# Optimization experiments

Hardware: AMD Instinct MI355X
Metric: run time of the kernel (lower is better)

The kernel has to match this reference:

```python
import jax, jax.numpy as jnp
import numpy as np

N, E, DIN, H, C = 50000, 800000, 256, 4, 32  # nodes, edges, in_dim, heads, per-head dim
NEG_SLOPE = 0.2  # PyG GATConv default LeakyReLU slope


def setup_inputs() -> dict:
    key = jax.random.key(0)
    ks = jax.random.split(key, 12)
    x = jax.random.normal(ks[0], (N, DIN), jnp.float32)
    edge_index = jax.random.randint(ks[1], (2, E), 0, N, dtype=jnp.int64)
    # layer 1: in=DIN -> heads*C; layer 2: in=H*C -> heads*C (concat=True default)
    W1 = jax.random.normal(ks[2], (DIN, H * C), jnp.float32) / np.sqrt(DIN).astype(np.float32)
    as1 = jax.random.normal(ks[3], (H, C), jnp.float32) * 0.1
    ad1 = jax.random.normal(ks[4], (H, C), jnp.float32) * 0.1
    b1 = jnp.zeros((H * C,), jnp.float32)
    W2 = jax.random.normal(ks[5], (H * C, H * C), jnp.float32) / np.sqrt(H * C).astype(np.float32)
    as2 = jax.random.normal(ks[6], (H, C), jnp.float32) * 0.1
    ad2 = jax.random.normal(ks[7], (H, C), jnp.float32) * 0.1
    b2 = jnp.zeros((H * C,), jnp.float32)
    return {"x": x, "edge_index": edge_index, "W1": W1, "as1": as1, "ad1": ad1,
            "b1": b1, "W2": W2, "as2": as2, "ad2": ad2, "b2": b2}


def gat_conv(x, src, dst, W, a_src, a_dst, b):
    # x: [N, Fin] -> h: [N, H, C]
    n = x.shape[0]
    h = (x @ W).reshape(n, H, C)
    # per-node attention logits [N, H]
    e_src = jnp.einsum('nhc,hc->nh', h, a_src)
    e_dst = jnp.einsum('nhc,hc->nh', h, a_dst)
    # edge-wise logits + segment softmax over destination neighborhoods
    e = jax.nn.leaky_relu(e_src[src] + e_dst[dst], NEG_SLOPE)  # [Et, H]
    m = jax.ops.segment_max(e, dst, num_segments=n)
    ex = jnp.exp(e - m[dst])
    s = jax.ops.segment_sum(ex, dst, num_segments=n)
    alpha = ex / s[dst]  # self-loops guarantee every node has >=1 edge
    # weighted scatter-add aggregation
    out = jax.ops.segment_sum(h[src] * alpha[:, :, None], dst, num_segments=n)
    return out.reshape(n, H * C) + b


def reference(x, edge_index, W1, as1, ad1, b1, W2, as2, ad2, b2):
    n = x.shape[0]
    loop = jnp.arange(n, dtype=edge_index.dtype)
    src = jnp.concatenate([edge_index[0], loop])  # PyG GATConv adds self-loops
    dst = jnp.concatenate([edge_index[1], loop])
    h = jax.nn.elu(gat_conv(x, src, dst, W1, as1, ad1, b1))
    # dropout is a no-op in eval mode (F.dropout with training=False)
    out = jax.nn.elu(gat_conv(h, src, dst, W2, as2, ad2, b2))
    return out
```

## Files before the change

### kernel.cpp

```cpp
#include <hip/hip_runtime.h>
#include <hip/hip_fp16.h>
#include <type_traits>

#define NN 50000
#define NE 800000
#define ET (NE + NN)
#define NEG 0.2f
#define GGRID 782
#define EGRID 3321

typedef __attribute__((ext_vector_type(4))) float f32x4;
typedef __attribute__((ext_vector_type(8))) short s16x8;

#define GLD_LDS16(g, l)                                                        \
  __builtin_amdgcn_global_load_lds(                                            \
      (const __attribute__((address_space(1))) void*)(g),                      \
      (__attribute__((address_space(3))) void*)(l), 16, 0, 0)

__device__ __forceinline__ float lrelu(float x) { return x > 0.0f ? x : NEG * x; }
__device__ __forceinline__ float elu1(float x) { return x > 0.0f ? x : __expf(x) - 1.0f; }
__device__ __forceinline__ unsigned short f2bf(float f) {
  unsigned u = __float_as_uint(f);
  u += 0x7FFFu + ((u >> 16) & 1u);
  return (unsigned short)(u >> 16);
}
__device__ __forceinline__ float bf2f(unsigned short h) {
  return __uint_as_float(((unsigned)h) << 16);
}

__global__ void prep_count_kernel(const float* __restrict__ W1, short* __restrict__ W1h,
                                  short* __restrict__ W1l, const float* __restrict__ W2,
                                  short* __restrict__ W2h, short* __restrict__ W2l,
                                  const int* __restrict__ ei, int* __restrict__ cnt,
                                  int* __restrict__ rank) {
  if (blockIdx.x >= 192) {
    int e = (blockIdx.x - 192) * 256 + threadIdx.x;
    if (e >= ET) return;
    int dst = (e < NE) ? ei[NE + e] : (e - NE);
    rank[e] = atomicAdd(&cnt[dst], 1);
    return;
  }
  int idx = blockIdx.x * 256 + threadIdx.x;
  const float* W; short* Wth; short* Wtl; int Kdim;
  if (idx < 256 * 128) { W = W1; Wth = W1h; Wtl = W1l; Kdim = 256; }
  else {
    idx -= 256 * 128;
    W = W2; Wth = W2h; Wtl = W2l; Kdim = 128;
  }
  int k = idx >> 7, n = idx & 127;
  float w = W[idx];
  unsigned short h = f2bf(w);
  unsigned short l = f2bf(w - bf2f(h));
  Wth[n * Kdim + k] = (short)h;
  Wtl[n * Kdim + k] = (short)l;
}

template<int K, typename AT>
__global__ __launch_bounds__(256) void gemm_mfma(const AT* __restrict__ A,
                                                 const short* __restrict__ Bth,
                                                 const short* __restrict__ Btl,
                                                 const float* __restrict__ a_s,
                                                 const float* __restrict__ a_d,
                                                 __half* __restrict__ outh,
                                                 float* __restrict__ es,
                                                 float* __restrict__ ed,
                                                 const int* __restrict__ ei,
                                                 const int* __restrict__ rowp,
                                                 const int* __restrict__ rank,
                                                 int* __restrict__ colw) {
  if (blockIdx.x >= GGRID) {
    int e = (blockIdx.x - GGRID) * 256 + threadIdx.x;
    if (e < ET) {
      int src, dst;
      if (e < NE) { src = ei[e]; dst = ei[NE + e]; } else { src = dst = e - NE; }
      colw[rowp[dst] + rank[e]] = src;
    }
    return;
  }
  constexpr int NSTEP = K / 32;
  __shared__ short Ah[64 * 32], Al[64 * 32];
  __shared__ short Bh[128 * 32], Bl[128 * 32];
  const int tid = threadIdx.x;
  const int lane = tid & 63;
  const int wv = tid >> 6;
  const int wm = wv >> 1, wn = wv & 1;
  const int row0 = blockIdx.x * 64;
  const int srow = tid >> 2;
  const int skc = tid & 3;

  f32x4 acc[2][4];
#pragma unroll
  for (int i = 0; i < 2; ++i)
#pragma unroll
    for (int j = 0; j < 4; ++j) acc[i][j] = (f32x4){0.f, 0.f, 0.f, 0.f};

  for (int s = 0; s < NSTEP; ++s) {
    __syncthreads();
    {
      int grow = row0 + srow; grow = grow < NN ? grow : NN - 1;
      const AT* ap = &A[(size_t)grow * K + s * 32 + skc * 8];
      float xs[8];
      if constexpr (std::is_same_v<AT, float>) {
        float4 x0 = *(const float4*)ap;
        float4 x1 = *(const float4*)(ap + 4);
        xs[0]=x0.x; xs[1]=x0.y; xs[2]=x0.z; xs[3]=x0.w;
        xs[4]=x1.x; xs[5]=x1.y; xs[6]=x1.z; xs[7]=x1.w;
      } else {
        int4 raw = *(const int4*)ap;
        const __half2* hv = (const __half2*)&raw;
#pragma unroll
        for (int q = 0; q < 4; ++q) {
          float2 f = __half22float2(hv[q]);
          xs[2 * q] = f.x; xs[2 * q + 1] = f.y;
        }
      }
      int hi[4], lo[4];
#pragma unroll
      for (int q = 0; q < 4; ++q) {
        unsigned short h0 = f2bf(xs[2 * q]);
        unsigned short l0 = f2bf(xs[2 * q] - bf2f(h0));
        unsigned short h1 = f2bf(xs[2 * q + 1]);
        unsigned short l1 = f2bf(xs[2 * q + 1] - bf2f(h1));
        hi[q] = (int)(((unsigned)h1 << 16) | h0);
        lo[q] = (int)(((unsigned)l1 << 16) | l0);
      }
      *(int4*)&Ah[srow * 32 + skc * 8] = make_int4(hi[0], hi[1], hi[2], hi[3]);
      *(int4*)&Al[srow * 32 + skc * 8] = make_int4(lo[0], lo[1], lo[2], lo[3]);
    }
#pragma unroll
    for (int rr = 0; rr < 2; ++rr) {
      int n = srow + rr * 64;
      const short* gh = &Bth[(size_t)n * K + s * 32 + skc * 8];
      const short* gl = &Btl[(size_t)n * K + s * 32 + skc * 8];
      char* lbh = (char*)Bh + rr * 4096 + wv * 1024;
      char* lbl = (char*)Bl + rr * 4096 + wv * 1024;
      GLD_LDS16(gh, lbh);
      GLD_LDS16(gl, lbl);
    }
    __syncthreads();
    const int fr = lane & 15;
    const int fk = (lane >> 4) * 8;
    s16x8 ah[2], al[2], bh[4], bl[4];
#pragma unroll
    for (int mf = 0; mf < 2; ++mf) {
      int r = wm * 32 + mf * 16 + fr;
      ah[mf] = *(const s16x8*)&Ah[r * 32 + fk];
      al[mf] = *(const s16x8*)&Al[r * 32 + fk];
    }
#pragma unroll
    for (int nf = 0; nf < 4; ++nf) {
      int n = wn * 64 + nf * 16 + fr;
      bh[nf] = *(const s16x8*)&Bh[n * 32 + fk];
      bl[nf] = *(const s16x8*)&Bl[n * 32 + fk];
    }
#pragma unroll
    for (int mf = 0; mf < 2; ++mf)
#pragma unroll
      for (int nf = 0; nf < 4; ++nf) {
        acc[mf][nf] = __builtin_amdgcn_mfma_f32_16x16x32_bf16(ah[mf], bh[nf], acc[mf][nf], 0, 0, 0);
        acc[mf][nf] = __builtin_amdgcn_mfma_f32_16x16x32_bf16(ah[mf], bl[nf], acc[mf][nf], 0, 0, 0);
        acc[mf][nf] = __builtin_amdgcn_mfma_f32_16x16x32_bf16(al[mf], bh[nf], acc[mf][nf], 0, 0, 0);
      }
  }

  const int fr = lane & 15;
  const int fg = lane >> 4;
  float asr[4], adr[4];
#pragma unroll
  for (int nf = 0; nf < 4; ++nf) {
    int c = wn * 64 + nf * 16 + fr;
    asr[nf] = a_s[c]; adr[nf] = a_d[c];
  }
#pragma unroll
  for (int mf = 0; mf < 2; ++mf) {
#pragma unroll
    for (int r = 0; r < 4; ++r) {
      int row = row0 + wm * 32 + mf * 16 + fg * 4 + r;
      float sp0 = acc[mf][0][r] * asr[0] + acc[mf][1][r] * asr[1];
      float sp1 = acc[mf][2][r] * asr[2] + acc[mf][3][r] * asr[3];
      float dp0 = acc[mf][0][r] * adr[0] + acc[mf][1][r] * adr[1];
      float dp1 = acc[mf][2][r] * adr[2] + acc[mf][3][r] * adr[3];
#pragma unroll
      for (int off = 1; off < 16; off <<= 1) {
        sp0 += __shfl_xor(sp0, off); sp1 += __shfl_xor(sp1, off);
        dp0 += __shfl_xor(dp0, off); dp1 += __shfl_xor(dp1, off);
      }
      if (row < NN) {
#pragma unroll
        for (int nf = 0; nf < 4; ++nf)
          outh[(size_t)row * 128 + wn * 64 + nf * 16 + fr] = __float2half(acc[mf][nf][r]);
        if (fr == 0) {
          es[row * 4 + wn * 2 + 0] = sp0;
          es[row * 4 + wn * 2 + 1] = sp1;
          ed[row * 4 + wn * 2 + 0] = dp0;
          ed[row * 4 + wn * 2 + 1] = dp1;
        }
      }
    }
  }
}

__global__ __launch_bounds__(1024) void scan_kernel(const int* __restrict__ cnt,
                                                    int* __restrict__ row_ptr, int n) {
  __shared__ int wsum[16];
  __shared__ int blocktot_s;
  __shared__ int carry_s;
  const int lane = threadIdx.x & 63;
  const int wv = threadIdx.x >> 6;
  if (threadIdx.x == 0) carry_s = 0;
  __syncthreads();
  for (int base = 0; base < n; base += 4096) {
    int idx = base + threadIdx.x * 4;
    int4 v = {0, 0, 0, 0};
    if (idx < n) v = *(const int4*)&cnt[idx];
    int tsum = v.x + v.y + v.z + v.w;
    int sc = tsum;
#pragma unroll
    for (int off = 1; off < 64; off <<= 1) {
      int t = __shfl_up(sc, off);
      if (lane >= off) sc += t;
    }
    if (lane == 63) wsum[wv] = sc;
    __syncthreads();
    if (wv == 0 && lane < 16) {
      int ws = wsum[lane];
      int si = ws;
#pragma unroll
      for (int off = 1; off < 16; off <<= 1) {
        int t = __shfl_up(si, off);
        if (lane >= off) si += t;
      }
      wsum[lane] = si - ws;
      if (lane == 15) blocktot_s = si;
    }
    __syncthreads();
    int run = carry_s + wsum[wv] + (sc - tsum);
    if (idx < n) {
      int4 o;
      o.x = run; o.y = run + v.x; o.z = o.y + v.y; o.w = o.z + v.z;
      *(int4*)&row_ptr[idx] = o;
    }
    __syncthreads();
    if (threadIdx.x == 0) carry_s += blocktot_s;
    __syncthreads();
  }
  if (threadIdx.x == 0) row_ptr[n] = carry_s;
}

template<typename OT>
__global__ __launch_bounds__(128) void agg_fused(const __half* __restrict__ h,
                                                 const float4* __restrict__ es4,
                                                 const float4* __restrict__ ed4,
                                                 const int* __restrict__ row_ptr,
                                                 const int* __restrict__ col,
                                                 const float* __restrict__ bias,
                                                 OT* __restrict__ out) {
  __shared__ float wc[2][512];
  __shared__ int   cc[2][128];
  int wid = (blockIdx.x * 128 + threadIdx.x) >> 6;
  if (wid >= NN) return;
  const int lane = threadIdx.x & 63;
  const int wv = (threadIdx.x >> 6) & 1;
  const int start = row_ptr[wid], end = row_ptr[wid + 1];
  const int deg = end - start;
  const float4 edv = ed4[wid];
  const char* hb = (const char*)h;

  const bool v0 = lane < deg, v1 = lane + 64 < deg;
  int c0 = 0, c1 = 0;
  float4 e0, e1;
  if (v0) { c0 = col[start + lane]; e0 = es4[c0]; }
  if (v1) { c1 = col[start + lane + 64]; e1 = es4[c1]; }
  float s0 = 0.f, s1 = 0.f, s2 = 0.f, s3 = 0.f;
  float4 p0, p1;
  if (v0) {
    p0.x = __expf(lrelu(e0.x + edv.x)); p0.y = __expf(lrelu(e0.y + edv.y));
    p0.z = __expf(lrelu(e0.z + edv.z)); p0.w = __expf(lrelu(e0.w + edv.w));
    s0 += p0.x; s1 += p0.y; s2 += p0.z; s3 += p0.w;
  }
  if (v1) {
    p1.x = __expf(lrelu(e1.x + edv.x)); p1.y = __expf(lrelu(e1.y + edv.y));
    p1.z = __expf(lrelu(e1.z + edv.z)); p1.w = __expf(lrelu(e1.w + edv.w));
    s0 += p1.x; s1 += p1.y; s2 += p1.z; s3 += p1.w;
  }
  for (int j = start + lane + 128; j < end; j += 64) {
    float4 ev = es4[col[j]];
    s0 += __expf(lrelu(ev.x + edv.x)); s1 += __expf(lrelu(ev.y + edv.y));
    s2 += __expf(lrelu(ev.z + edv.z)); s3 += __expf(lrelu(ev.w + edv.w));
  }
#pragma unroll
  for (int off = 32; off; off >>= 1) {
    s0 += __shfl_xor(s0, off); s1 += __shfl_xor(s1, off);
    s2 += __shfl_xor(s2, off); s3 += __shfl_xor(s3, off);
  }
  const float i0 = 1.0f / s0, i1 = 1.0f / s1, i2 = 1.0f / s2, i3 = 1.0f / s3;
  if (v0) {
    float4 w; w.x = p0.x * i0; w.y = p0.y * i1; w.z = p0.z * i2; w.w = p0.w * i3;
    *(float4*)&wc[wv][lane * 4] = w;
    cc[wv][lane] = c0 << 8;
  }
  if (v1) {
    float4 w; w.x = p1.x * i0; w.y = p1.y * i1; w.z = p1.z * i2; w.w = p1.w * i3;
    *(float4*)&wc[wv][(lane + 64) * 4] = w;
    cc[wv][lane + 64] = c1 << 8;
  }
  const int deg1 = deg < 128 ? deg : 128;
  if (lane == 0 && (deg1 & 1)) {
    cc[wv][deg1] = cc[wv][0];
    float4 z = {0.f, 0.f, 0.f, 0.f};
    *(float4*)&wc[wv][deg1 * 4] = z;
  }

  const int half_ = lane >> 5;
  const int fl = lane & 31;
  const int hd2 = fl >> 3;
  const int fb = fl << 3;
  float a0 = 0.f, a1 = 0.f, a2 = 0.f, a3 = 0.f;
  const int degR = (deg1 + 1) & ~1;
  int jj = 0;
  for (; jj + 8 <= degR; jj += 8) {
    int off[4]; float w[4];
#pragma unroll
    for (int u = 0; u < 4; ++u) {
      int e = jj + 2 * u + half_;
      off[u] = cc[wv][e];
      w[u] = wc[wv][e * 4 + hd2];
    }
    int2 q[4];
#pragma unroll
    for (int u = 0; u < 4; ++u) q[u] = *(const int2*)(hb + off[u] + fb);
#pragma unroll
    for (int u = 0; u < 4; ++u) {
      float2 f0 = __half22float2(*(const __half2*)&q[u].x);
      float2 f1 = __half22float2(*(const __half2*)&q[u].y);
      a0 = fmaf(f0.x, w[u], a0); a1 = fmaf(f0.y, w[u], a1);
      a2 = fmaf(f1.x, w[u], a2); a3 = fmaf(f1.y, w[u], a3);
    }
  }
  for (; jj < degR; jj += 2) {
    int e = jj + half_;
    int off = cc[wv][e];
    float w = wc[wv][e * 4 + hd2];
    int2 q = *(const int2*)(hb + off + fb);
    float2 f0 = __half22float2(*(const __half2*)&q.x);
    float2 f1 = __half22float2(*(const __half2*)&q.y);
    a0 = fmaf(f0.x, w, a0); a1 = fmaf(f0.y, w, a1);
    a2 = fmaf(f1.x, w, a2); a3 = fmaf(f1.y, w, a3);
  }
  if (deg > 128) {
    float ih = hd2 == 0 ? i0 : hd2 == 1 ? i1 : hd2 == 2 ? i2 : i3;
    float eh = hd2 == 0 ? edv.x : hd2 == 1 ? edv.y : hd2 == 2 ? edv.z : edv.w;
    for (int j = start + 128 + half_; j < end; j += 2) {
      int t = col[j];
      const float* ep = (const float*)&es4[t];
      float w = __expf(lrelu(ep[hd2] + eh)) * ih;
      int2 q = *(const int2*)(hb + (t << 8) + fb);
      float2 f0 = __half22float2(*(const __half2*)&q.x);
      float2 f1 = __half22float2(*(const __half2*)&q.y);
      a0 = fmaf(f0.x, w, a0); a1 = fmaf(f0.y, w, a1);
      a2 = fmaf(f1.x, w, a2); a3 = fmaf(f1.y, w, a3);
    }
  }
  a0 += __shfl_xor(a0, 32); a1 += __shfl_xor(a1, 32);
  a2 += __shfl_xor(a2, 32); a3 += __shfl_xor(a3, 32);

  float4 bs = *(const float4*)&bias[fl * 4];
  if (half_ == 0) {
    float o0 = elu1(a0 + bs.x), o1 = elu1(a1 + bs.y);
    float o2 = elu1(a2 + bs.z), o3 = elu1(a3 + bs.w);
    if constexpr (std::is_same_v<OT, float>) {
      float4 o; o.x = o0; o.y = o1; o.z = o2; o.w = o3;
      *(float4*)&out[(size_t)wid * 128 + fl * 4] = o;
    } else {
      __half2 h01 = __floats2half2_rn(o0, o1);
      __half2 h23 = __floats2half2_rn(o2, o3);
      int2 pk; pk.x = *(int*)&h01; pk.y = *(int*)&h23;
      *(int2*)&out[(size_t)wid * 128 + fl * 4] = pk;
    }
  }
}

extern "C" void kernel_launch(void* const* d_in, const int* in_sizes, int n_in,
                              void* d_out, int out_size, void* d_ws, size_t ws_size,
                              hipStream_t stream) {
  const float* x   = (const float*)d_in[0];
  const int*   ei  = (const int*)d_in[1];
  const float* W1  = (const float*)d_in[2];
  const float* as1 = (const float*)d_in[3];
  const float* ad1 = (const float*)d_in[4];
  const float* b1  = (const float*)d_in[5];
  const float* W2  = (const float*)d_in[6];
  const float* as2 = (const float*)d_in[7];
  const float* ad2 = (const float*)d_in[8];
  const float* b2  = (const float*)d_in[9];

  char* ws = (char*)d_ws;
  __half* h     = (__half*)(ws);
  __half* h2    = (__half*)(ws + 12800000);
  float*  es    = (float*) (ws + 25600000);
  float*  ed    = (float*) (ws + 26400000);
  int*    cnt   = (int*)   (ws + 27200000);
  int*    rowp  = (int*)   (ws + 27400000);
  int*    col   = (int*)   (ws + 27600064);
  int*    rank  = (int*)   (ws + 31000064);
  short*  wt1h  = (short*) (ws + 34400064);
  short*  wt1l  = (short*) (ws + 34465600);
  short*  wt2h  = (short*) (ws + 34531136);
  short*  wt2l  = (short*) (ws + 34563904);

  hipMemsetAsync(cnt, 0, NN * sizeof(int), stream);

  prep_count_kernel<<<192 + EGRID, 256, 0, stream>>>(W1, wt1h, wt1l, W2, wt2h, wt2l,
                                                     ei, cnt, rank);

  scan_kernel<<<1, 1024, 0, stream>>>(cnt, rowp, NN);

  int ngrid = (NN + 1) / 2;

  gemm_mfma<256, float><<<GGRID + EGRID, 256, 0, stream>>>(
      x, wt1h, wt1l, as1, ad1, h, es, ed, ei, rowp, rank, col);

  agg_fused<__half><<<ngrid, 128, 0, stream>>>(h, (const float4*)es, (const float4*)ed,
                                               rowp, col, b1, h2);

  gemm_mfma<128, __half><<<GGRID, 256, 0, stream>>>(
      h2, wt2h, wt2l, as2, ad2, h, es, ed, nullptr, nullptr, nullptr, nullptr);
  agg_fused<float><<<ngrid, 128, 0, stream>>>(h, (const float4*)es, (const float4*)ed,
                                              rowp, col, b2, (float*)d_out);
}
```

Measured before the change: 181.5 us.

## Drop LDS staging in MFMA GEMM; each wave loads fragments directly from global

```diff
diff --git a/kernel.cpp b/kernel.cpp
--- a/kernel.cpp
+++ b/kernel.cpp
@@ -6,16 +6,11 @@
 #define NE 800000
 #define ET (NE + NN)
 #define NEG 0.2f
-#define GGRID 782
+#define GG2 1563
 #define EGRID 3321
 
 typedef __attribute__((ext_vector_type(4))) float f32x4;
 typedef __attribute__((ext_vector_type(8))) short s16x8;
-
-#define GLD_LDS16(g, l)                                                        \
-  __builtin_amdgcn_global_load_lds(                                            \
-      (const __attribute__((address_space(1))) void*)(g),                      \
-      (__attribute__((address_space(3))) void*)(l), 16, 0, 0)
 
 __device__ __forceinline__ float lrelu(float x) { return x > 0.0f ? x : NEG * x; }
 __device__ __forceinline__ float elu1(float x) { return x > 0.0f ? x : __expf(x) - 1.0f; }
@@ -68,8 +63,8 @@
                                                  const int* __restrict__ rowp,
                                                  const int* __restrict__ rank,
                                                  int* __restrict__ colw) {
-  if (blockIdx.x >= GGRID) {
-    int e = (blockIdx.x - GGRID) * 256 + threadIdx.x;
+  if (blockIdx.x >= GG2) {
+    int e = (blockIdx.x - GG2) * 256 + threadIdx.x;
     if (e < ET) {
       int src, dst;
       if (e < NE) { src = ei[e]; dst = ei[NE + e]; } else { src = dst = e - NE; }
@@ -78,93 +73,63 @@
     return;
   }
   constexpr int NSTEP = K / 32;
-  __shared__ short Ah[64 * 32], Al[64 * 32];
-  __shared__ short Bh[128 * 32], Bl[128 * 32];
   const int tid = threadIdx.x;
   const int lane = tid & 63;
-  const int wv = tid >> 6;
-  const int wm = wv >> 1, wn = wv & 1;
-  const int row0 = blockIdx.x * 64;
-  const int srow = tid >> 2;
-  const int skc = tid & 3;
-
-  f32x4 acc[2][4];
-#pragma unroll
-  for (int i = 0; i < 2; ++i)
-#pragma unroll
-    for (int j = 0; j < 4; ++j) acc[i][j] = (f32x4){0.f, 0.f, 0.f, 0.f};
-
-  for (int s = 0; s < NSTEP; ++s) {
-    __syncthreads();
-    {
-      int grow = row0 + srow; grow = grow < NN ? grow : NN - 1;
-      const AT* ap = &A[(size_t)grow * K + s * 32 + skc * 8];
-      float xs[8];
-      if constexpr (std::is_same_v<AT, float>) {
-        float4 x0 = *(const float4*)ap;
-        float4 x1 = *(const float4*)(ap + 4);
-        xs[0]=x0.x; xs[1]=x0.y; xs[2]=x0.z; xs[3]=x0.w;
-        xs[4]=x1.x; xs[5]=x1.y; xs[6]=x1.z; xs[7]=x1.w;
-      } else {
-        int4 raw = *(const int4*)ap;
-        const __half2* hv = (const __half2*)&raw;
-#pragma unroll
-        for (int q = 0; q < 4; ++q) {
-          float2 f = __half22float2(hv[q]);
-          xs[2 * q] = f.x; xs[2 * q + 1] = f.y;
-        }
-      }
-      int hi[4], lo[4];
-#pragma unroll
-      for (int q = 0; q < 4; ++q) {
-        unsigned short h0 = f2bf(xs[2 * q]);
-        unsigned short l0 = f2bf(xs[2 * q] - bf2f(h0));
-        unsigned short h1 = f2bf(xs[2 * q + 1]);
-        unsigned short l1 = f2bf(xs[2 * q + 1] - bf2f(h1));
-        hi[q] = (int)(((unsigned)h1 << 16) | h0);
-        lo[q] = (int)(((unsigned)l1 << 16) | l0);
-      }
-      *(int4*)&Ah[srow * 32 + skc * 8] = make_int4(hi[0], hi[1], hi[2], hi[3]);
-      *(int4*)&Al[srow * 32 + skc * 8] = make_int4(lo[0], lo[1], lo[2], lo[3]);
-    }
-#pragma unroll
-    for (int rr = 0; rr < 2; ++rr) {
-      int n = srow + rr * 64;
-      const short* gh = &Bth[(size_t)n * K + s * 32 + skc * 8];
-      const short* gl = &Btl[(size_t)n * K + s * 32 + skc * 8];
-      char* lbh = (char*)Bh + rr * 4096 + wv * 1024;
-      char* lbl = (char*)Bl + rr * 4096 + wv * 1024;
-      GLD_LDS16(gh, lbh);
-      GLD_LDS16(gl, lbl);
-    }
-    __syncthreads();
-    const int fr = lane & 15;
-    const int fk = (lane >> 4) * 8;
-    s16x8 ah[2], al[2], bh[4], bl[4];
-#pragma unroll
-    for (int mf = 0; mf < 2; ++mf) {
-      int r = wm * 32 + mf * 16 + fr;
-      ah[mf] = *(const s16x8*)&Ah[r * 32 + fk];
-      al[mf] = *(const s16x8*)&Al[r * 32 + fk];
-    }
-#pragma unroll
-    for (int nf = 0; nf < 4; ++nf) {
-      int n = wn * 64 + nf * 16 + fr;
-      bh[nf] = *(const s16x8*)&Bh[n * 32 + fk];
-      bl[nf] = *(const s16x8*)&Bl[n * 32 + fk];
-    }
-#pragma unroll
-    for (int mf = 0; mf < 2; ++mf)
-#pragma unroll
-      for (int nf = 0; nf < 4; ++nf) {
-        acc[mf][nf] = __builtin_amdgcn_mfma_f32_16x16x32_bf16(ah[mf], bh[nf], acc[mf][nf], 0, 0, 0);
-        acc[mf][nf] = __builtin_amdgcn_mfma_f32_16x16x32_bf16(ah[mf], bl[nf], acc[mf][nf], 0, 0, 0);
-        acc[mf][nf] = __builtin_amdgcn_mfma_f32_16x16x32_bf16(al[mf], bh[nf], acc[mf][nf], 0, 0, 0);
-      }
-  }
-
   const int fr = lane & 15;
   const int fg = lane >> 4;
+  const int gw = blockIdx.x * 4 + (tid >> 6);
+  const int rt = gw >> 1;
+  const int wn = gw & 1;
+  int arow = rt * 16 + fr;
+  const int arowc = arow < NN ? arow : NN - 1;
+
+  f32x4 acc[4];
+#pragma unroll
+  for (int j = 0; j < 4; ++j) acc[j] = (f32x4){0.f, 0.f, 0.f, 0.f};
+
+  const AT* aptr = &A[(size_t)arowc * K + fg * 8];
+  const short* bhp = &Bth[(size_t)(wn * 64 + fr) * K + fg * 8];
+  const short* blp = &Btl[(size_t)(wn * 64 + fr) * K + fg * 8];
+
+#pragma unroll 2
+  for (int s = 0; s < NSTEP; ++s) {
+    float xs[8];
+    if constexpr (std::is_same_v<AT, float>) {
+      float4 x0 = *(const float4*)(aptr + s * 32);
+      float4 x1 = *(const float4*)(aptr + s * 32 + 4);
+      xs[0]=x0.x; xs[1]=x0.y; xs[2]=x0.z; xs[3]=x0.w;
+      xs[4]=x1.x; xs[5]=x1.y; xs[6]=x1.z; xs[7]=x1.w;
+    } else {
+      int4 raw = *(const int4*)(aptr + s * 32);
+      const __half2* hv = (const __half2*)&raw;
+#pragma unroll
+      for (int q = 0; q < 4; ++q) {
+        float2 f = __half22float2(hv[q]);
+        xs[2 * q] = f.x; xs[2 * q + 1] = f.y;
+      }
+    }
+    s16x8 ah, al;
+#pragma unroll
+    for (int q = 0; q < 8; ++q) {
+      unsigned short h = f2bf(xs[q]);
+      unsigned short l = f2bf(xs[q] - bf2f(h));
+      ah[q] = (short)h;
+      al[q] = (short)l;
+    }
+    s16x8 bh[4], bl[4];
+#pragma unroll
+    for (int nf = 0; nf < 4; ++nf) {
+      bh[nf] = *(const s16x8*)(bhp + (size_t)nf * 16 * K + s * 32);
+      bl[nf] = *(const s16x8*)(blp + (size_t)nf * 16 * K + s * 32);
+    }
+#pragma unroll
+    for (int nf = 0; nf < 4; ++nf) {
+      acc[nf] = __builtin_amdgcn_mfma_f32_16x16x32_bf16(ah, bh[nf], acc[nf], 0, 0, 0);
+      acc[nf] = __builtin_amdgcn_mfma_f32_16x16x32_bf16(ah, bl[nf], acc[nf], 0, 0, 0);
+      acc[nf] = __builtin_amdgcn_mfma_f32_16x16x32_bf16(al, bh[nf], acc[nf], 0, 0, 0);
+    }
+  }
+
   float asr[4], adr[4];
 #pragma unroll
   for (int nf = 0; nf < 4; ++nf) {
@@ -172,29 +137,26 @@
     asr[nf] = a_s[c]; adr[nf] = a_d[c];
   }
 #pragma unroll
-  for (int mf = 0; mf < 2; ++mf) {
-#pragma unroll
-    for (int r = 0; r < 4; ++r) {
-      int row = row0 + wm * 32 + mf * 16 + fg * 4 + r;
-      float sp0 = acc[mf][0][r] * asr[0] + acc[mf][1][r] * asr[1];
-      float sp1 = acc[mf][2][r] * asr[2] + acc[mf][3][r] * asr[3];
-      float dp0 = acc[mf][0][r] * adr[0] + acc[mf][1][r] * adr[1];
-      float dp1 = acc[mf][2][r] * adr[2] + acc[mf][3][r] * adr[3];
-#pragma unroll
-      for (int off = 1; off < 16; off <<= 1) {
-        sp0 += __shfl_xor(sp0, off); sp1 += __shfl_xor(sp1, off);
-        dp0 += __shfl_xor(dp0, off); dp1 += __shfl_xor(dp1, off);
-      }
-      if (row < NN) {
-#pragma unroll
-        for (int nf = 0; nf < 4; ++nf)
-          outh[(size_t)row * 128 + wn * 64 + nf * 16 + fr] = __float2half(acc[mf][nf][r]);
-        if (fr == 0) {
-          es[row * 4 + wn * 2 + 0] = sp0;
-          es[row * 4 + wn * 2 + 1] = sp1;
-          ed[row * 4 + wn * 2 + 0] = dp0;
-          ed[row * 4 + wn * 2 + 1] = dp1;
-        }
+  for (int r = 0; r < 4; ++r) {
+    int row = rt * 16 + fg * 4 + r;
+    float sp0 = acc[0][r] * asr[0] + acc[1][r] * asr[1];
+    float sp1 = acc[2][r] * asr[2] + acc[3][r] * asr[3];
+    float dp0 = acc[0][r] * adr[0] + acc[1][r] * adr[1];
+    float dp1 = acc[2][r] * adr[2] + acc[3][r] * adr[3];
+#pragma unroll
+    for (int off = 1; off < 16; off <<= 1) {
+      sp0 += __shfl_xor(sp0, off); sp1 += __shfl_xor(sp1, off);
+      dp0 += __shfl_xor(dp0, off); dp1 += __shfl_xor(dp1, off);
+    }
+    if (row < NN) {
+#pragma unroll
+      for (int nf = 0; nf < 4; ++nf)
+        outh[(size_t)row * 128 + wn * 64 + nf * 16 + fr] = __float2half(acc[nf][r]);
+      if (fr == 0) {
+        es[row * 4 + wn * 2 + 0] = sp0;
+        es[row * 4 + wn * 2 + 1] = sp1;
+        ed[row * 4 + wn * 2 + 0] = dp0;
+        ed[row * 4 + wn * 2 + 1] = dp1;
       }
     }
   }
@@ -417,13 +379,13 @@
 
   int ngrid = (NN + 1) / 2;
 
-  gemm_mfma<256, float><<<GGRID + EGRID, 256, 0, stream>>>(
+  gemm_mfma<256, float><<<GG2 + EGRID, 256, 0, stream>>>(
       x, wt1h, wt1l, as1, ad1, h, es, ed, ei, rowp, rank, col);
 
   agg_fused<__half><<<ngrid, 128, 0, stream>>>(h, (const float4*)es, (const float4*)ed,
                                                rowp, col, b1, h2);
 
-  gemm_mfma<128, __half><<<GGRID, 256, 0, stream>>>(
+  gemm_mfma<128, __half><<<GG2, 256, 0, stream>>>(
       h2, wt2h, wt2l, as2, ad2, h, es, ed, nullptr, nullptr, nullptr, nullptr);
   agg_fused<float><<<ngrid, 128, 0, stream>>>(h, (const float4*)es, (const float4*)ed,
                                               rowp, col, b2, (float*)d_out);
```

After: 239.5 us. 1.32x slower.
